# Kernel optimization log

Measured on AMD Instinct MI355X. Metric: run time of the kernel, lower is better.

The kernel has to match this reference:

```python
import jax, jax.numpy as jnp
import numpy as np

B, NCLS, T, D, L = 32, 20, 2048, 2048, 128
GAMMA = 0.1           # maxGamma temperature
THRES = 0.5           # lcs threshold
FEAT_MARGIN = 50.0
LAMB1, LAMB2, LAMB3 = 1.0, 5e-5, 2e-4
LAMB_LCS, LAMB_FSD = 0.1, 0.1


def _similarity(a, b):
    # row-normalized cosine similarity: [L, d] x [L, d] -> [L, L]
    a = a / jnp.linalg.norm(a, axis=1, keepdims=True)
    b = b / jnp.linalg.norm(b, axis=1, keepdims=True)
    return a @ b.T


def _fsd_dp(m, g):
    # soft-DP: C[i,j] = m[i-1,j-1] + gamma*logsumexp([C[i-1,j-1], g+C[i-1,j], g+C[i,j-1]]/gamma)
    n = m.shape[0]
    def row_step(prev_row, rows):          # prev_row: C[i-1, 0..n]
        m_row, g_row = rows
        def col_step(c_left, xs):
            c_diag, c_up, m_ij, g_ij = xs
            neigh = jnp.stack([c_diag, g_ij + c_up, g_ij + c_left])
            new = m_ij + GAMMA * jax.nn.logsumexp(neigh / GAMMA)
            return new, new
        _, vals = jax.lax.scan(col_step, jnp.zeros((), m.dtype),
                               (prev_row[:-1], prev_row[1:], m_row, g_row))
        new_row = jnp.concatenate([jnp.zeros((1,), m.dtype), vals])
        return new_row, None
    final_row, _ = jax.lax.scan(row_step, jnp.zeros((n + 1,), m.dtype), (m, g))
    return final_row[-1]


def _lcs_dp(s):
    # C[i,j] = C[i-1,j-1]+s if s>thres else max(C[i-1,j], C[i,j-1])
    n = s.shape[0]
    def row_step(prev_row, s_row):
        def col_step(c_left, xs):
            c_diag, c_up, s_ij = xs
            new = jnp.where(s_ij > THRES, c_diag + s_ij, jnp.maximum(c_up, c_left))
            return new, new
        _, vals = jax.lax.scan(col_step, jnp.zeros((), s.dtype),
                               (prev_row[:-1], prev_row[1:], s_row))
        return jnp.concatenate([jnp.zeros((1,), s.dtype), vals]), None
    final_row, _ = jax.lax.scan(row_step, jnp.zeros((n + 1,), s.dtype), s)
    return final_row[-1]


def _fsd_pair(c0, c1):
    h = c0.shape[-1] // 2
    m = _similarity(c0[:, :h], c1[:, :h])
    g = _similarity(c0[:, h:], c1[:, h:])
    return _fsd_dp(m, g)


def _lcs_pair(c0, c1):
    sim = _similarity(c0, c1)
    s = jnp.maximum(0.0, sim - 0.8) * 5.0
    return _lcs_dp(s)


def _cls_criterion(x, lab):
    return -jnp.mean(jnp.sum(jnp.log(x + 1e-45) * lab, axis=1))


def _acm_forward(act_inst_cls, act_cont_cls, act_back_cls, vid_label, temp_att,
                 act_inst_feat, act_cont_feat, act_back_feat, temp_cas,
                 lcs_candi, fsd_act_candi, fsd_bak_candi, pos_pair, neg_pair):
    bsz = act_inst_cls.shape[0]
    zeros = jnp.zeros((bsz, 1), act_inst_cls.dtype)
    ones = jnp.ones((bsz, 1), act_inst_cls.dtype)
    inst_lab = jnp.concatenate([vid_label, zeros], axis=1)
    cont_lab = jnp.concatenate([vid_label, ones], axis=1)
    back_lab = jnp.concatenate([jnp.zeros_like(vid_label), ones], axis=1)
    inst_lab = inst_lab / jnp.sum(inst_lab, axis=1, keepdims=True)
    cont_lab = cont_lab / jnp.sum(cont_lab, axis=1, keepdims=True)
    back_lab = back_lab / jnp.sum(back_lab, axis=1, keepdims=True)
    cls_loss = (_cls_criterion(act_inst_cls, inst_lab)
                + _cls_criterion(act_cont_cls, cont_lab)
                + _cls_criterion(act_back_cls, back_lab))

    guide_loss = jnp.mean(jnp.sum(jnp.abs(
        1.0 - temp_cas[:, :, -1] - jax.lax.stop_gradient(temp_att[:, :, 0])), axis=1))

    n_i = jnp.linalg.norm(act_inst_feat, axis=1)
    n_c = jnp.linalg.norm(act_cont_feat, axis=1)
    n_b = jnp.linalg.norm(act_back_feat, axis=1)
    f1 = jnp.maximum(FEAT_MARGIN - n_i + n_c, 0.0)
    f2 = jnp.maximum(FEAT_MARGIN - n_c + n_b, 0.0)
    feat_loss = jnp.mean((f1 + f2 + n_b) ** 2)

    sparse_loss = jnp.mean(jnp.sum(temp_att[:, :, :2], axis=1))

    acm_loss = cls_loss + LAMB1 * guide_loss + LAMB2 * feat_loss + LAMB3 * sparse_loss

    # LCS branch (pairs are constants)
    pos_lcs = jax.vmap(_lcs_pair)(lcs_candi[pos_pair[:, 0]], lcs_candi[pos_pair[:, 1]]).mean()
    neg_lcs = jax.vmap(_lcs_pair)(lcs_candi[neg_pair[:, 0]], lcs_candi[neg_pair[:, 1]]).mean()
    lcs_loss = neg_lcs - pos_lcs

    # FSD branch
    act_act = jax.vmap(_fsd_pair)(fsd_act_candi[pos_pair[:, 0]], fsd_act_candi[pos_pair[:, 1]]).mean()
    act_bak = jax.vmap(_fsd_pair)(fsd_act_candi[neg_pair[:, 0]], fsd_bak_candi[neg_pair[:, 1]]).mean()
    fsd_loss = act_bak - act_act

    return acm_loss + LAMB_LCS * lcs_loss + LAMB_FSD * fsd_loss


def setup_inputs() -> dict:
    key = jax.random.key(0)
    ks = jax.random.split(key, 12)
    # single-label videos: 16 classes, each appearing twice -> 16 pos pairs
    classes = np.arange(B) % 16
    vid_label = jnp.asarray(np.eye(NCLS, dtype=np.float32)[classes])
    pos_pair = jnp.asarray(np.stack([np.arange(16), np.arange(16) + 16], axis=1).astype(np.int32))
    neg_pair = jnp.asarray(np.stack([np.arange(16), np.arange(16) + 1], axis=1).astype(np.int32))
    return {
        "act_inst_cls": jax.random.uniform(ks[0], (B, NCLS + 1), jnp.float32),
        "act_cont_cls": jax.random.uniform(ks[1], (B, NCLS + 1), jnp.float32),
        "act_back_cls": jax.random.uniform(ks[2], (B, NCLS + 1), jnp.float32),
        "vid_label": vid_label,
        "temp_att": jax.random.uniform(ks[3], (B, T, 3), jnp.float32),
        "act_inst_feat": jax.random.normal(ks[4], (B, D), jnp.float32),
        "act_cont_feat": jax.random.normal(ks[5], (B, D), jnp.float32),
        "act_back_feat": jax.random.normal(ks[6], (B, D), jnp.float32),
        "temp_cas": jax.random.uniform(ks[7], (B, T, NCLS + 1), jnp.float32),
        "lcs_candi": jax.random.normal(ks[8], (B, L, D), jnp.float32),
        "fsd_act_candi": jax.random.normal(ks[9], (B, L, D), jnp.float32),
        "fsd_bak_candi": jax.random.normal(ks[10], (B, L, D), jnp.float32),
        "pos_pair": pos_pair,
        "neg_pair": neg_pair,
    }


def reference(act_inst_cls, act_cont_cls, act_back_cls, vid_label, temp_att,
              act_inst_feat, act_cont_feat, act_back_feat, temp_cas,
              lcs_candi, fsd_act_candi, fsd_bak_candi, pos_pair, neg_pair):
    return _acm_forward(act_inst_cls, act_cont_cls, act_back_cls, vid_label, temp_att,
                        act_inst_feat, act_cont_feat, act_back_feat, temp_cas,
                        lcs_candi, fsd_act_candi, fsd_bak_candi, pos_pair, neg_pair)
```

## Files before the change

kernel.cpp:

```cpp
#include <hip/hip_runtime.h>
#include <hip/hip_bf16.h>
#include <math.h>

#define B_    32
#define NCLS_ 20
#define T_    2048
#define D_    2048
#define L_    128
#define NPAIR 16

#define OFF_LCS_PART 0
#define OFF_M_PART   2097152
#define OFF_G_PART   3145728
#define OFF_RN       4194304
#define OFF_NFEAT    4214784
#define OFF_LCS_RES  4214880
#define OFF_FSD_RES  4214912
#define OFF_ACC      4214944
#define SLICE_STRIDE 524288

typedef __attribute__((ext_vector_type(8))) short bf16x8;
typedef __attribute__((ext_vector_type(4))) float f32x4;

__device__ __forceinline__ ushort f2bf(float f) {
    __hip_bfloat16 h = __float2bfloat16(f);
    return *reinterpret_cast<ushort*>(&h);
}

__global__ __launch_bounds__(64) void norm_guide_kernel(
        const float* __restrict__ lcs, const float* __restrict__ fa,
        const float* __restrict__ fb, const float* __restrict__ fi,
        const float* __restrict__ fc, const float* __restrict__ fbk,
        const float* __restrict__ att, const float* __restrict__ cas,
        float* __restrict__ ws) {
    __shared__ float sc[64 * 21 + 64 * 3];
    int b = blockIdx.x;
    int tid = threadIdx.x;

    if (b >= 20576) {
        float* sa = sc + 64 * 21;
        size_t e0 = (size_t)(b - 20576) * 64;
        const float4* pc = (const float4*)(cas + e0 * 21);
        #pragma unroll
        for (int i = 0; i < 6; ++i) {
            int idx = tid + i * 64;
            if (idx < 336) *(float4*)&sc[idx * 4] = pc[idx];
        }
        const float4* pa = (const float4*)(att + e0 * 3);
        if (tid < 48) *(float4*)&sa[tid * 4] = pa[tid];
        __syncthreads();
        float a0 = sa[tid * 3], a1 = sa[tid * 3 + 1];
        float g = fabsf(1.f - sc[tid * 21 + 20] - a0);
        float sp = a0 + a1;
        #pragma unroll
        for (int off = 32; off; off >>= 1) {
            g += __shfl_down(g, off);
            sp += __shfl_down(sp, off);
        }
        if (tid == 0) {
            atomicAdd(&ws[OFF_ACC + 0], g);
            atomicAdd(&ws[OFF_ACC + 1], sp);
        }
        return;
    }

    const float* src; float* dst; int len4; int recip = 1;
    float* rn = ws + OFF_RN;
    if (b < 4096) {
        src = lcs + (size_t)b * 2048; dst = rn + b; len4 = 512;
    } else if (b < 20480) {
        int region = (b - 4096) >> 12;
        int r = (b - 4096) & 4095;
        const float* base = (region < 2) ? fa : fb;
        src = base + (size_t)r * 2048 + (region & 1) * 1024;
        dst = rn + b; len4 = 256;
    } else {
        int r = b - 20480;
        const float* base = (r < 32) ? fi : (r < 64 ? fc : fbk);
        src = base + (size_t)(r & 31) * 2048;
        dst = ws + OFF_NFEAT + r; len4 = 512; recip = 0;
    }
    const float4* p = (const float4*)src;
    float s = 0.f;
    for (int i = tid; i < len4; i += 64) {
        float4 v = p[i];
        s += v.x * v.x + v.y * v.y + v.z * v.z + v.w * v.w;
    }
    #pragma unroll
    for (int off = 32; off; off >>= 1) s += __shfl_down(s, off);
    if (tid == 0) *dst = recip ? rsqrtf(s) : sqrtf(s);
}

__global__ __launch_bounds__(256) void sim_mfma_kernel(
        const float* __restrict__ lcs, const float* __restrict__ fa,
        const float* __restrict__ fb, const int* __restrict__ pos,
        const int* __restrict__ neg, float* __restrict__ ws) {
    int bid = blockIdx.x;
    const float *Aptr, *Bptr;
    float* out;

    if (bid < 128) {
        int job = bid >> 2, ks = bid & 3;
        int pi = job & 15;
        const int* pp = (job >= 16) ? neg : pos;
        int p0 = pp[2 * pi], p1 = pp[2 * pi + 1];
        Aptr = lcs + (size_t)p0 * L_ * D_ + ks * 512;
        Bptr = lcs + (size_t)p1 * L_ * D_ + ks * 512;
        out = ws + OFF_LCS_PART + ((size_t)ks * 32 + job) * 16384;
    } else {
        int e = bid - 128;
        int fj = e >> 1, ks = e & 1;
        int isneg = fj >= 32;
        int q = fj & 31;
        int pi = q >> 1, half = q & 1;
        const int* pp = isneg ? neg : pos;
        int p0 = pp[2 * pi], p1 = pp[2 * pi + 1];
        const float* Bbase = isneg ? fb : fa;
        Aptr = fa + (size_t)p0 * L_ * D_ + half * 1024 + ks * 512;
        Bptr = Bbase + (size_t)p1 * L_ * D_ + half * 1024 + ks * 512;
        int slot = (isneg ? 16 : 0) + pi;
        out = ws + (half ? OFF_G_PART : OFF_M_PART) + ((size_t)ks * 32 + slot) * 16384;
    }

    __shared__ ushort lA[2][128 * 64];
    __shared__ ushort lB[2][128 * 64];
    int tid = threadIdx.x;
    int lane = tid & 63;
    int w = tid >> 6;
    int wr = w >> 1, wc = w & 1;
    int lrow = lane & 15, lhk = lane >> 4;

    int srow[4], skb[4];
    #pragma unroll
    for (int i = 0; i < 4; ++i) {
        int c = tid + i * 256;
        srow[i] = c >> 3; skb[i] = c & 7;
    }

    float4 pa0[4], pa1[4], pb0[4], pb1[4];

    f32x4 acc[4][4];
    #pragma unroll
    for (int m = 0; m < 4; ++m)
        #pragma unroll
        for (int n = 0; n < 4; ++n)
            acc[m][n] = (f32x4){0.f, 0.f, 0.f, 0.f};

    #pragma unroll
    for (int i = 0; i < 4; ++i) {
        const float* sA = Aptr + (size_t)srow[i] * D_ + skb[i] * 8;
        pa0[i] = *(const float4*)sA; pa1[i] = *(const float4*)(sA + 4);
        const float* sB = Bptr + (size_t)srow[i] * D_ + skb[i] * 8;
        pb0[i] = *(const float4*)sB; pb1[i] = *(const float4*)(sB + 4);
    }
    #pragma unroll
    for (int i = 0; i < 4; ++i) {
        int idx = ((srow[i] * 64 + skb[i] * 8) ^ ((srow[i] & 7) << 3));
        bf16x8 sv, sw;
        sv[0] = (short)f2bf(pa0[i].x); sv[1] = (short)f2bf(pa0[i].y);
        sv[2] = (short)f2bf(pa0[i].z); sv[3] = (short)f2bf(pa0[i].w);
        sv[4] = (short)f2bf(pa1[i].x); sv[5] = (short)f2bf(pa1[i].y);
        sv[6] = (short)f2bf(pa1[i].z); sv[7] = (short)f2bf(pa1[i].w);
        *(bf16x8*)&lA[0][idx] = sv;
        sw[0] = (short)f2bf(pb0[i].x); sw[1] = (short)f2bf(pb0[i].y);
        sw[2] = (short)f2bf(pb0[i].z); sw[3] = (short)f2bf(pb0[i].w);
        sw[4] = (short)f2bf(pb1[i].x); sw[5] = (short)f2bf(pb1[i].y);
        sw[6] = (short)f2bf(pb1[i].z); sw[7] = (short)f2bf(pb1[i].w);
        *(bf16x8*)&lB[0][idx] = sw;
    }
    __syncthreads();

    #pragma unroll
    for (int t = 0; t < 8; ++t) {
        if (t < 7) {
            int k0 = (t + 1) * 64;
            #pragma unroll
            for (int i = 0; i < 4; ++i) {
                const float* sA = Aptr + (size_t)srow[i] * D_ + k0 + skb[i] * 8;
                pa0[i] = *(const float4*)sA; pa1[i] = *(const float4*)(sA + 4);
                const float* sB = Bptr + (size_t)srow[i] * D_ + k0 + skb[i] * 8;
                pb0[i] = *(const float4*)sB; pb1[i] = *(const float4*)(sB + 4);
            }
        }
        #pragma unroll
        for (int ks = 0; ks < 2; ++ks) {
            int kbase = ks * 32 + lhk * 8;
            bf16x8 afr[4], bfr[4];
            #pragma unroll
            for (int m = 0; m < 4; ++m) {
                int row = wr * 64 + m * 16 + lrow;
                int idx = ((row * 64 + kbase) ^ ((row & 7) << 3));
                afr[m] = *(const bf16x8*)&lA[t & 1][idx];
            }
            #pragma unroll
            for (int n = 0; n < 4; ++n) {
                int row = wc * 64 + n * 16 + lrow;
                int idx = ((row * 64 + kbase) ^ ((row & 7) << 3));
                bfr[n] = *(const bf16x8*)&lB[t & 1][idx];
            }
            #pragma unroll
            for (int m = 0; m < 4; ++m)
                #pragma unroll
                for (int n = 0; n < 4; ++n)
                    acc[m][n] = __builtin_amdgcn_mfma_f32_16x16x32_bf16(
                        afr[m], bfr[n], acc[m][n], 0, 0, 0);
        }
        if (t < 7) {
            #pragma unroll
            for (int i = 0; i < 4; ++i) {
                int idx = ((srow[i] * 64 + skb[i] * 8) ^ ((srow[i] & 7) << 3));
                bf16x8 sv, sw;
                sv[0] = (short)f2bf(pa0[i].x); sv[1] = (short)f2bf(pa0[i].y);
                sv[2] = (short)f2bf(pa0[i].z); sv[3] = (short)f2bf(pa0[i].w);
                sv[4] = (short)f2bf(pa1[i].x); sv[5] = (short)f2bf(pa1[i].y);
                sv[6] = (short)f2bf(pa1[i].z); sv[7] = (short)f2bf(pa1[i].w);
                *(bf16x8*)&lA[(t + 1) & 1][idx] = sv;
                sw[0] = (short)f2bf(pb0[i].x); sw[1] = (short)f2bf(pb0[i].y);
                sw[2] = (short)f2bf(pb0[i].z); sw[3] = (short)f2bf(pb0[i].w);
                sw[4] = (short)f2bf(pb1[i].x); sw[5] = (short)f2bf(pb1[i].y);
                sw[6] = (short)f2bf(pb1[i].z); sw[7] = (short)f2bf(pb1[i].w);
                *(bf16x8*)&lB[(t + 1) & 1][idx] = sw;
            }
        }
        __syncthreads();
    }

    #pragma unroll
    for (int m = 0; m < 4; ++m) {
        #pragma unroll
        for (int n = 0; n < 4; ++n) {
            int jj = wc * 64 + n * 16 + lrow;
            #pragma unroll
            for (int r = 0; r < 4; ++r) {
                int ii = wr * 64 + m * 16 + lhk * 4 + r;
                out[ii * L_ + jj] = acc[m][n][r];
            }
        }
    }
}

__global__ __launch_bounds__(256) void dp_kernel(const int* __restrict__ pos,
                                                 const int* __restrict__ neg,
                                                 float* __restrict__ ws) {
    __shared__ float Sm[128 * 128];
    __shared__ float Sg[128 * 128];
    int job = blockIdx.x;
    int tid = threadIdx.x;
    const float* rn = ws + OFF_RN;
    bool is_lcs = job < 32;

    if (is_lcs) {
        int pi = job & 15;
        const int* pp = (job >= 16) ? neg : pos;
        int p0 = pp[2 * pi], p1 = pp[2 * pi + 1];
        const float* P = ws + OFF_LCS_PART + (size_t)job * 16384;
        const float* rA = rn + p0 * 128;
        const float* rB = rn + p1 * 128;
        #pragma unroll
        for (int c = 0; c < 16; ++c) {
            int base = (c * 256 + tid) * 4;
            int r = base >> 7, j0 = base & 127;
            float4 v0 = *(const float4*)&P[base];
            float4 v1 = *(const float4*)&P[SLICE_STRIDE + base];
            float4 v2 = *(const float4*)&P[2 * SLICE_STRIDE + base];
            float4 v3 = *(const float4*)&P[3 * SLICE_STRIDE + base];
            float ra = rA[r];
            float4 rb = *(const float4*)&rB[j0];
            float4 sv;
            sv.x = fmaxf(((v0.x + v1.x + v2.x + v3.x) * ra * rb.x - 0.8f) * 5.f, 0.f);
            sv.y = fmaxf(((v0.y + v1.y + v2.y + v3.y) * ra * rb.y - 0.8f) * 5.f, 0.f);
            sv.z = fmaxf(((v0.z + v1.z + v2.z + v3.z) * ra * rb.z - 0.8f) * 5.f, 0.f);
            sv.w = fmaxf(((v0.w + v1.w + v2.w + v3.w) * ra * rb.w - 0.8f) * 5.f, 0.f);
            *(float4*)&Sm[base] = sv;
        }
    } else {
        int fj = job - 32;
        int isneg = fj >= 16;
        int pi = fj & 15;
        const int* pp = isneg ? neg : pos;
        int p0 = pp[2 * pi], p1 = pp[2 * pi + 1];
        const float* Pm = ws + OFF_M_PART + (size_t)fj * 16384;
        const float* Pg = ws + OFF_G_PART + (size_t)fj * 16384;
        const float* rAm = rn + 4096 + p0 * 128;
        const float* rBm = rn + (isneg ? 12288 : 4096) + p1 * 128;
        const float* rAg = rn + 8192 + p0 * 128;
        const float* rBg = rn + (isneg ? 16384 : 8192) + p1 * 128;
        #pragma unroll
        for (int c = 0; c < 16; ++c) {
            int base = (c * 256 + tid) * 4;
            int r = base >> 7, j0 = base & 127;
            float4 m0 = *(const float4*)&Pm[base];
            float4 m1 = *(const float4*)&Pm[SLICE_STRIDE + base];
            float4 g0 = *(const float4*)&Pg[base];
            float4 g1 = *(const float4*)&Pg[SLICE_STRIDE + base];
            float ram = rAm[r], rag = rAg[r];
            float4 rbm = *(const float4*)&rBm[j0];
            float4 rbg = *(const float4*)&rBg[j0];
            float4 mv, gv;
            mv.x = (m0.x + m1.x) * ram * rbm.x;
            mv.y = (m0.y + m1.y) * ram * rbm.y;
            mv.z = (m0.z + m1.z) * ram * rbm.z;
            mv.w = (m0.w + m1.w) * ram * rbm.w;
            gv.x = (g0.x + g1.x) * rag * rbg.x;
            gv.y = (g0.y + g1.y) * rag * rbg.y;
            gv.z = (g0.z + g1.z) * rag * rbg.z;
            gv.w = (g0.w + g1.w) * rag * rbg.w;
            *(float4*)&Sm[base] = mv;
            *(float4*)&Sg[base] = gv;
        }
    }
    __syncthreads();

    if (tid >= 64) return;
    int l = tid;
    const float* SA = Sm + l * 128;
    const float* SB = Sm + (64 + l) * 128;
    float a = 0.f, b = 0.f, ua_prev = 0.f, ub_prev = 0.f;

    if (is_lcs) {
        float sa_buf[4], sb_buf[4];
        #pragma unroll
        for (int p = 0; p < 4; ++p) {
            sa_buf[p] = SA[min(max(p - l, 0), 127)];
            sb_buf[p] = SB[min(max(p - 64 - l, 0), 127)];
        }
        #pragma unroll 4
        for (int t = 0; t < 256; ++t) {
            int slot = t & 3;
            float sa = sa_buf[slot], sb = sb_buf[slot];
            float ua = __shfl_up(a, 1);
            float a63 = __shfl(a, 63);
            float ub = __shfl_up(b, 1);
            if (l == 0) { ua = 0.f; ub = a63; }
            int ja = t - l, jb = t - 64 - l;
            float newa = (sa > 0.5f) ? (ua_prev + sa) : fmaxf(ua, a);
            float newb = (sb > 0.5f) ? (ub_prev + sb) : fmaxf(ub, b);
            if (ja >= 0 && ja < 128) a = newa;
            if (jb >= 0 && jb < 128) b = newb;
            ua_prev = ua; ub_prev = ub;
            sa_buf[slot] = SA[min(max(t + 4 - l, 0), 127)];
            sb_buf[slot] = SB[min(max(t + 4 - 64 - l, 0), 127)];
        }
        if (l == 63) ws[OFF_LCS_RES + job] = b;
    } else {
        const float* GA = Sg + l * 128;
        const float* GB = Sg + (64 + l) * 128;
        float mab[4], gab[4], mbb[4], gbb[4];
        #pragma unroll
        for (int p = 0; p < 4; ++p) {
            int ja = min(max(p - l, 0), 127), jb = min(max(p - 64 - l, 0), 127);
            mab[p] = SA[ja]; gab[p] = GA[ja];
            mbb[p] = SB[jb]; gbb[p] = GB[jb];
        }
        #pragma unroll 4
        for (int t = 0; t < 256; ++t) {
            int slot = t & 3;
            float ma = mab[slot], ga = gab[slot], mb = mbb[slot], gb = gbb[slot];
            float ua = __shfl_up(a, 1);
            float a63 = __shfl(a, 63);
            float ub = __shfl_up(b, 1);
            if (l == 0) { ua = 0.f; ub = a63; }
            int ja = t - l, jb = t - 64 - l;
            float x0 = ua_prev, x1 = ga + ua, x2 = ga + a;
            float mx = fmaxf(x0, fmaxf(x1, x2));
            float e0 = __expf((x0 - mx) * 10.f);
            float e1 = __expf((x1 - mx) * 10.f);
            float e2 = __expf((x2 - mx) * 10.f);
            float newa = ma + mx + 0.1f * __logf(e0 + e1 + e2);
            float y0 = ub_prev, y1 = gb + ub, y2 = gb + b;
            float my = fmaxf(y0, fmaxf(y1, y2));
            float f0 = __expf((y0 - my) * 10.f);
            float f1 = __expf((y1 - my) * 10.f);
            float f2 = __expf((y2 - my) * 10.f);
            float newb = mb + my + 0.1f * __logf(f0 + f1 + f2);
            if (ja >= 0 && ja < 128) a = newa;
            if (jb >= 0 && jb < 128) b = newb;
            ua_prev = ua; ub_prev = ub;
            int jan = min(max(t + 4 - l, 0), 127), jbn = min(max(t + 4 - 64 - l, 0), 127);
            mab[slot] = SA[jan]; gab[slot] = GA[jan];
            mbb[slot] = SB[jbn]; gbb[slot] = GB[jbn];
        }
        if (l == 63) ws[OFF_FSD_RES + (job - 32)] = b;
    }
}

__global__ __launch_bounds__(64) void final_kernel(const float* __restrict__ xi,
                                                   const float* __restrict__ xc,
                                                   const float* __restrict__ xb,
                                                   const float* __restrict__ vl,
                                                   const float* __restrict__ ws,
                                                   float* __restrict__ out) {
    const float* nfeat = ws + OFF_NFEAT;
    const float* lcs_res = ws + OFF_LCS_RES;
    const float* fsd_res = ws + OFF_FSD_RES;
    const float* acc = ws + OFF_ACC;
    int lane = threadIdx.x;
    float part = 0.f;

    if (lane < B_) {
        int b = lane;
        float sv = 0.f;
        for (int j = 0; j < NCLS_; ++j) sv += vl[b * NCLS_ + j];
        float inv_i = 1.f / sv;
        float inv_c = 1.f / (sv + 1.f);
        float si = 0.f, sc = 0.f;
        for (int j = 0; j < NCLS_; ++j) {
            float lab = vl[b * NCLS_ + j];
            if (lab != 0.f) {
                si += logf(xi[b * (NCLS_ + 1) + j] + 1e-45f) * lab * inv_i;
                sc += logf(xc[b * (NCLS_ + 1) + j] + 1e-45f) * lab * inv_c;
            }
        }
        sc += logf(xc[b * (NCLS_ + 1) + NCLS_] + 1e-45f) * inv_c;
        float sb = logf(xb[b * (NCLS_ + 1) + NCLS_] + 1e-45f);
        float cls = -(si + sc + sb) / (float)B_;

        float ni = nfeat[b], nc = nfeat[B_ + b], nb = nfeat[2 * B_ + b];
        float f1 = fmaxf(50.f - ni + nc, 0.f);
        float f2 = fmaxf(50.f - nc + nb, 0.f);
        float fv = f1 + f2 + nb;
        float feat = fv * fv / (float)B_;

        float sgn = (b < NPAIR) ? -1.f : 1.f;
        float lcs = sgn * lcs_res[b] / (float)NPAIR;
        float fsd = sgn * fsd_res[b] / (float)NPAIR;

        part = cls + 5e-5f * feat + 0.1f * (lcs + fsd);
    }
    #pragma unroll
    for (int off = 32; off; off >>= 1) part += __shfl_down(part, off);
    if (lane == 0) {
        float guide = acc[0] / (float)B_;
        float sparse = acc[1] / (float)B_;
        out[0] = part + guide + 2e-4f * sparse;
    }
}

extern "C" void kernel_launch(void* const* d_in, const int* in_sizes, int n_in,
                              void* d_out, int out_size, void* d_ws, size_t ws_size,
                              hipStream_t stream) {
    const float* act_inst_cls = (const float*)d_in[0];
    const float* act_cont_cls = (const float*)d_in[1];
    const float* act_back_cls = (const float*)d_in[2];
    const float* vid_label    = (const float*)d_in[3];
    const float* temp_att     = (const float*)d_in[4];
    const float* act_inst_feat= (const float*)d_in[5];
    const float* act_cont_feat= (const float*)d_in[6];
    const float* act_back_feat= (const float*)d_in[7];
    const float* temp_cas     = (const float*)d_in[8];
    const float* lcs_candi    = (const float*)d_in[9];
    const float* fsd_act      = (const float*)d_in[10];
    const float* fsd_bak      = (const float*)d_in[11];
    const int*   pos_pair     = (const int*)d_in[12];
    const int*   neg_pair     = (const int*)d_in[13];

    float* ws = (float*)d_ws;
    float* out = (float*)d_out;

    hipMemsetAsync(ws + OFF_ACC, 0, 2 * sizeof(float), stream);

    hipLaunchKernelGGL(sim_mfma_kernel, dim3(256), dim3(256), 0, stream,
                       lcs_candi, fsd_act, fsd_bak, pos_pair, neg_pair, ws);

    hipLaunchKernelGGL(norm_guide_kernel, dim3(21600), dim3(64), 0, stream,
                       lcs_candi, fsd_act, fsd_bak,
                       act_inst_feat, act_cont_feat, act_back_feat,
                       temp_att, temp_cas, ws);

    hipLaunchKernelGGL(dp_kernel, dim3(64), dim3(256), 0, stream,
                       pos_pair, neg_pair, ws);

    hipLaunchKernelGGL(final_kernel, dim3(1), dim3(64), 0, stream,
                       act_inst_cls, act_cont_cls, act_back_cls, vid_label,
                       ws, out);
}
```

Baseline: 269.7 us.

## Raise split-K factor for similarity GEMMs and use DPP shifts in DP wavefront

When the workspace is large enough, the similarity GEMM is split over twice as many K slices (8 for LCS, 4 for FSD). This doubles the number of blocks to fill more CUs, at the cost of more partial buffers for the DP kernel to read and sum. The DP wavefront loop now uses DPP row shifts and readlane in place of generic shuffles, and its LDS prefetch depth goes from 4 to 8 slots. Workspace offsets are now computed on the host from the split factors instead of fixed defines.

```diff
diff --git a/kernel.cpp b/kernel.cpp
--- a/kernel.cpp
+++ b/kernel.cpp
@@ -8,15 +8,6 @@
 #define D_    2048
 #define L_    128
 #define NPAIR 16
-
-#define OFF_LCS_PART 0
-#define OFF_M_PART   2097152
-#define OFF_G_PART   3145728
-#define OFF_RN       4194304
-#define OFF_NFEAT    4214784
-#define OFF_LCS_RES  4214880
-#define OFF_FSD_RES  4214912
-#define OFF_ACC      4214944
 #define SLICE_STRIDE 524288
 
 typedef __attribute__((ext_vector_type(8))) short bf16x8;
@@ -25,6 +16,24 @@
 __device__ __forceinline__ ushort f2bf(float f) {
     __hip_bfloat16 h = __float2bfloat16(f);
     return *reinterpret_cast<ushort*>(&h);
+}
+
+__device__ __forceinline__ float wave_shr1(float x) {
+#if __has_builtin(__builtin_amdgcn_update_dpp)
+    int r = __builtin_amdgcn_update_dpp(0, __builtin_bit_cast(int, x),
+                                        0x138 , 0xf, 0xf, true);
+    return __builtin_bit_cast(float, r);
+#else
+    return __shfl_up(x, 1);
+#endif
+}
+__device__ __forceinline__ float rdlane63(float x) {
+#if __has_builtin(__builtin_amdgcn_readlane)
+    return __builtin_bit_cast(float,
+        __builtin_amdgcn_readlane(__builtin_bit_cast(int, x), 63));
+#else
+    return __shfl(x, 63);
+#endif
 }
 
 __global__ __launch_bounds__(64) void norm_guide_kernel(
@@ -32,7 +41,8 @@
         const float* __restrict__ fb, const float* __restrict__ fi,
         const float* __restrict__ fc, const float* __restrict__ fbk,
         const float* __restrict__ att, const float* __restrict__ cas,
-        float* __restrict__ ws) {
+        float* __restrict__ rn, float* __restrict__ nfeat,
+        float* __restrict__ acc) {
     __shared__ float sc[64 * 21 + 64 * 3];
     int b = blockIdx.x;
     int tid = threadIdx.x;
@@ -58,14 +68,13 @@
             sp += __shfl_down(sp, off);
         }
         if (tid == 0) {
-            atomicAdd(&ws[OFF_ACC + 0], g);
-            atomicAdd(&ws[OFF_ACC + 1], sp);
+            atomicAdd(&acc[0], g);
+            atomicAdd(&acc[1], sp);
         }
         return;
     }
 
     const float* src; float* dst; int len4; int recip = 1;
-    float* rn = ws + OFF_RN;
     if (b < 4096) {
         src = lcs + (size_t)b * 2048; dst = rn + b; len4 = 512;
     } else if (b < 20480) {
@@ -78,7 +87,7 @@
         int r = b - 20480;
         const float* base = (r < 32) ? fi : (r < 64 ? fc : fbk);
         src = base + (size_t)(r & 31) * 2048;
-        dst = ws + OFF_NFEAT + r; len4 = 512; recip = 0;
+        dst = nfeat + r; len4 = 512; recip = 0;
     }
     const float4* p = (const float4*)src;
     float s = 0.f;
@@ -94,32 +103,39 @@
 __global__ __launch_bounds__(256) void sim_mfma_kernel(
         const float* __restrict__ lcs, const float* __restrict__ fa,
         const float* __restrict__ fb, const int* __restrict__ pos,
-        const int* __restrict__ neg, float* __restrict__ ws) {
+        const int* __restrict__ neg, float* __restrict__ lcs_part,
+        float* __restrict__ m_part, float* __restrict__ g_part,
+        int sl, int sf) {
     int bid = blockIdx.x;
     const float *Aptr, *Bptr;
     float* out;
-
-    if (bid < 128) {
-        int job = bid >> 2, ks = bid & 3;
+    int nst;
+
+    if (bid < 32 * sl) {
+        int job = bid / sl, ks = bid - job * sl;
+        int kofs = ks * (2048 / sl);
+        nst = 2048 / (64 * sl);
         int pi = job & 15;
         const int* pp = (job >= 16) ? neg : pos;
         int p0 = pp[2 * pi], p1 = pp[2 * pi + 1];
-        Aptr = lcs + (size_t)p0 * L_ * D_ + ks * 512;
-        Bptr = lcs + (size_t)p1 * L_ * D_ + ks * 512;
-        out = ws + OFF_LCS_PART + ((size_t)ks * 32 + job) * 16384;
+        Aptr = lcs + (size_t)p0 * L_ * D_ + kofs;
+        Bptr = lcs + (size_t)p1 * L_ * D_ + kofs;
+        out = lcs_part + ((size_t)ks * 32 + job) * 16384;
     } else {
-        int e = bid - 128;
-        int fj = e >> 1, ks = e & 1;
+        int e = bid - 32 * sl;
+        int fj = e / sf, ks = e - fj * sf;
+        int kofs = ks * (1024 / sf);
+        nst = 1024 / (64 * sf);
         int isneg = fj >= 32;
         int q = fj & 31;
         int pi = q >> 1, half = q & 1;
         const int* pp = isneg ? neg : pos;
         int p0 = pp[2 * pi], p1 = pp[2 * pi + 1];
         const float* Bbase = isneg ? fb : fa;
-        Aptr = fa + (size_t)p0 * L_ * D_ + half * 1024 + ks * 512;
-        Bptr = Bbase + (size_t)p1 * L_ * D_ + half * 1024 + ks * 512;
+        Aptr = fa + (size_t)p0 * L_ * D_ + half * 1024 + kofs;
+        Bptr = Bbase + (size_t)p1 * L_ * D_ + half * 1024 + kofs;
         int slot = (isneg ? 16 : 0) + pi;
-        out = ws + (half ? OFF_G_PART : OFF_M_PART) + ((size_t)ks * 32 + slot) * 16384;
+        out = (half ? g_part : m_part) + ((size_t)ks * 32 + slot) * 16384;
     }
 
     __shared__ ushort lA[2][128 * 64];
@@ -170,9 +186,8 @@
     }
     __syncthreads();
 
-    #pragma unroll
-    for (int t = 0; t < 8; ++t) {
-        if (t < 7) {
+    for (int t = 0; t < nst; ++t) {
+        if (t < nst - 1) {
             int k0 = (t + 1) * 64;
             #pragma unroll
             for (int i = 0; i < 4; ++i) {
@@ -205,7 +220,7 @@
                     acc[m][n] = __builtin_amdgcn_mfma_f32_16x16x32_bf16(
                         afr[m], bfr[n], acc[m][n], 0, 0, 0);
         }
-        if (t < 7) {
+        if (t < nst - 1) {
             #pragma unroll
             for (int i = 0; i < 4; ++i) {
                 int idx = ((srow[i] * 64 + skb[i] * 8) ^ ((srow[i] & 7) << 3));
@@ -239,38 +254,40 @@
     }
 }
 
-__global__ __launch_bounds__(256) void dp_kernel(const int* __restrict__ pos,
-                                                 const int* __restrict__ neg,
-                                                 float* __restrict__ ws) {
+__global__ __launch_bounds__(256) void dp_kernel(
+        const int* __restrict__ pos, const int* __restrict__ neg,
+        const float* __restrict__ lcs_part, const float* __restrict__ m_part,
+        const float* __restrict__ g_part, const float* __restrict__ rn,
+        float* __restrict__ lres, float* __restrict__ fres,
+        int sl, int sf) {
     __shared__ float Sm[128 * 128];
     __shared__ float Sg[128 * 128];
     int job = blockIdx.x;
     int tid = threadIdx.x;
-    const float* rn = ws + OFF_RN;
     bool is_lcs = job < 32;
 
     if (is_lcs) {
         int pi = job & 15;
         const int* pp = (job >= 16) ? neg : pos;
         int p0 = pp[2 * pi], p1 = pp[2 * pi + 1];
-        const float* P = ws + OFF_LCS_PART + (size_t)job * 16384;
+        const float* P = lcs_part + (size_t)job * 16384;
         const float* rA = rn + p0 * 128;
         const float* rB = rn + p1 * 128;
-        #pragma unroll
         for (int c = 0; c < 16; ++c) {
             int base = (c * 256 + tid) * 4;
             int r = base >> 7, j0 = base & 127;
-            float4 v0 = *(const float4*)&P[base];
-            float4 v1 = *(const float4*)&P[SLICE_STRIDE + base];
-            float4 v2 = *(const float4*)&P[2 * SLICE_STRIDE + base];
-            float4 v3 = *(const float4*)&P[3 * SLICE_STRIDE + base];
+            float4 sacc = {0.f, 0.f, 0.f, 0.f};
+            for (int s = 0; s < sl; ++s) {
+                float4 v = *(const float4*)&P[(size_t)s * SLICE_STRIDE + base];
+                sacc.x += v.x; sacc.y += v.y; sacc.z += v.z; sacc.w += v.w;
+            }
             float ra = rA[r];
             float4 rb = *(const float4*)&rB[j0];
             float4 sv;
-            sv.x = fmaxf(((v0.x + v1.x + v2.x + v3.x) * ra * rb.x - 0.8f) * 5.f, 0.f);
-            sv.y = fmaxf(((v0.y + v1.y + v2.y + v3.y) * ra * rb.y - 0.8f) * 5.f, 0.f);
-            sv.z = fmaxf(((v0.z + v1.z + v2.z + v3.z) * ra * rb.z - 0.8f) * 5.f, 0.f);
-            sv.w = fmaxf(((v0.w + v1.w + v2.w + v3.w) * ra * rb.w - 0.8f) * 5.f, 0.f);
+            sv.x = fmaxf((sacc.x * ra * rb.x - 0.8f) * 5.f, 0.f);
+            sv.y = fmaxf((sacc.y * ra * rb.y - 0.8f) * 5.f, 0.f);
+            sv.z = fmaxf((sacc.z * ra * rb.z - 0.8f) * 5.f, 0.f);
+            sv.w = fmaxf((sacc.w * ra * rb.w - 0.8f) * 5.f, 0.f);
             *(float4*)&Sm[base] = sv;
         }
     } else {
@@ -279,32 +296,30 @@
         int pi = fj & 15;
         const int* pp = isneg ? neg : pos;
         int p0 = pp[2 * pi], p1 = pp[2 * pi + 1];
-        const float* Pm = ws + OFF_M_PART + (size_t)fj * 16384;
-        const float* Pg = ws + OFF_G_PART + (size_t)fj * 16384;
+        const float* Pm = m_part + (size_t)fj * 16384;
+        const float* Pg = g_part + (size_t)fj * 16384;
         const float* rAm = rn + 4096 + p0 * 128;
         const float* rBm = rn + (isneg ? 12288 : 4096) + p1 * 128;
         const float* rAg = rn + 8192 + p0 * 128;
         const float* rBg = rn + (isneg ? 16384 : 8192) + p1 * 128;
-        #pragma unroll
         for (int c = 0; c < 16; ++c) {
             int base = (c * 256 + tid) * 4;
             int r = base >> 7, j0 = base & 127;
-            float4 m0 = *(const float4*)&Pm[base];
-            float4 m1 = *(const float4*)&Pm[SLICE_STRIDE + base];
-            float4 g0 = *(const float4*)&Pg[base];
-            float4 g1 = *(const float4*)&Pg[SLICE_STRIDE + base];
+            float4 macc = {0.f, 0.f, 0.f, 0.f}, gacc = {0.f, 0.f, 0.f, 0.f};
+            for (int s = 0; s < sf; ++s) {
+                float4 m = *(const float4*)&Pm[(size_t)s * SLICE_STRIDE + base];
+                float4 g = *(const float4*)&Pg[(size_t)s * SLICE_STRIDE + base];
+                macc.x += m.x; macc.y += m.y; macc.z += m.z; macc.w += m.w;
+                gacc.x += g.x; gacc.y += g.y; gacc.z += g.z; gacc.w += g.w;
+            }
             float ram = rAm[r], rag = rAg[r];
             float4 rbm = *(const float4*)&rBm[j0];
             float4 rbg = *(const float4*)&rBg[j0];
             float4 mv, gv;
-            mv.x = (m0.x + m1.x) * ram * rbm.x;
-            mv.y = (m0.y + m1.y) * ram * rbm.y;
-            mv.z = (m0.z + m1.z) * ram * rbm.z;
-            mv.w = (m0.w + m1.w) * ram * rbm.w;
-            gv.x = (g0.x + g1.x) * rag * rbg.x;
-            gv.y = (g0.y + g1.y) * rag * rbg.y;
-            gv.z = (g0.z + g1.z) * rag * rbg.z;
-            gv.w = (g0.w + g1.w) * rag * rbg.w;
+            mv.x = macc.x * ram * rbm.x; mv.y = macc.y * ram * rbm.y;
+            mv.z = macc.z * ram * rbm.z; mv.w = macc.w * ram * rbm.w;
+            gv.x = gacc.x * rag * rbg.x; gv.y = gacc.y * rag * rbg.y;
+            gv.z = gacc.z * rag * rbg.z; gv.w = gacc.w * rag * rbg.w;
             *(float4*)&Sm[base] = mv;
             *(float4*)&Sg[base] = gv;
         }
@@ -318,19 +333,19 @@
     float a = 0.f, b = 0.f, ua_prev = 0.f, ub_prev = 0.f;
 
     if (is_lcs) {
-        float sa_buf[4], sb_buf[4];
-        #pragma unroll
-        for (int p = 0; p < 4; ++p) {
+        float sa_buf[8], sb_buf[8];
+        #pragma unroll
+        for (int p = 0; p < 8; ++p) {
             sa_buf[p] = SA[min(max(p - l, 0), 127)];
             sb_buf[p] = SB[min(max(p - 64 - l, 0), 127)];
         }
-        #pragma unroll 4
+        #pragma unroll 8
         for (int t = 0; t < 256; ++t) {
-            int slot = t & 3;
+            int slot = t & 7;
             float sa = sa_buf[slot], sb = sb_buf[slot];
-            float ua = __shfl_up(a, 1);
-            float a63 = __shfl(a, 63);
-            float ub = __shfl_up(b, 1);
+            float ua = wave_shr1(a);
+            float ub = wave_shr1(b);
+            float a63 = rdlane63(a);
             if (l == 0) { ua = 0.f; ub = a63; }
             int ja = t - l, jb = t - 64 - l;
             float newa = (sa > 0.5f) ? (ua_prev + sa) : fmaxf(ua, a);
@@ -338,27 +353,27 @@
             if (ja >= 0 && ja < 128) a = newa;
             if (jb >= 0 && jb < 128) b = newb;
             ua_prev = ua; ub_prev = ub;
-            sa_buf[slot] = SA[min(max(t + 4 - l, 0), 127)];
-            sb_buf[slot] = SB[min(max(t + 4 - 64 - l, 0), 127)];
-        }
-        if (l == 63) ws[OFF_LCS_RES + job] = b;
+            sa_buf[slot] = SA[min(max(t + 8 - l, 0), 127)];
+            sb_buf[slot] = SB[min(max(t + 8 - 64 - l, 0), 127)];
+        }
+        if (l == 63) lres[job] = b;
     } else {
         const float* GA = Sg + l * 128;
         const float* GB = Sg + (64 + l) * 128;
-        float mab[4], gab[4], mbb[4], gbb[4];
-        #pragma unroll
-        for (int p = 0; p < 4; ++p) {
+        float mab[8], gab[8], mbb[8], gbb[8];
+        #pragma unroll
+        for (int p = 0; p < 8; ++p) {
             int ja = min(max(p - l, 0), 127), jb = min(max(p - 64 - l, 0), 127);
             mab[p] = SA[ja]; gab[p] = GA[ja];
             mbb[p] = SB[jb]; gbb[p] = GB[jb];
         }
-        #pragma unroll 4
+        #pragma unroll 8
         for (int t = 0; t < 256; ++t) {
-            int slot = t & 3;
+            int slot = t & 7;
             float ma = mab[slot], ga = gab[slot], mb = mbb[slot], gb = gbb[slot];
-            float ua = __shfl_up(a, 1);
-            float a63 = __shfl(a, 63);
-            float ub = __shfl_up(b, 1);
+            float ua = wave_shr1(a);
+            float ub = wave_shr1(b);
+            float a63 = rdlane63(a);
             if (l == 0) { ua = 0.f; ub = a63; }
             int ja = t - l, jb = t - 64 - l;
             float x0 = ua_prev, x1 = ga + ua, x2 = ga + a;
@@ -376,24 +391,20 @@
             if (ja >= 0 && ja < 128) a = newa;
             if (jb >= 0 && jb < 128) b = newb;
             ua_prev = ua; ub_prev = ub;
-            int jan = min(max(t + 4 - l, 0), 127), jbn = min(max(t + 4 - 64 - l, 0), 127);
+            int jan = min(max(t + 8 - l, 0), 127), jbn = min(max(t + 8 - 64 - l, 0), 127);
             mab[slot] = SA[jan]; gab[slot] = GA[jan];
             mbb[slot] = SB[jbn]; gbb[slot] = GB[jbn];
         }
-        if (l == 63) ws[OFF_FSD_RES + (job - 32)] = b;
-    }
-}
-
-__global__ __launch_bounds__(64) void final_kernel(const float* __restrict__ xi,
-                                                   const float* __restrict__ xc,
-                                                   const float* __restrict__ xb,
-                                                   const float* __restrict__ vl,
-                                                   const float* __restrict__ ws,
-                                                   float* __restrict__ out) {
-    const float* nfeat = ws + OFF_NFEAT;
-    const float* lcs_res = ws + OFF_LCS_RES;
-    const float* fsd_res = ws + OFF_FSD_RES;
-    const float* acc = ws + OFF_ACC;
+        if (l == 63) fres[job - 32] = b;
+    }
+}
+
+__global__ __launch_bounds__(64) void final_kernel(
+        const float* __restrict__ xi, const float* __restrict__ xc,
+        const float* __restrict__ xb, const float* __restrict__ vl,
+        const float* __restrict__ nfeat, const float* __restrict__ lcs_res,
+        const float* __restrict__ fsd_res, const float* __restrict__ acc,
+        float* __restrict__ out) {
     int lane = threadIdx.x;
     float part = 0.f;
 
@@ -457,20 +468,40 @@
     float* ws = (float*)d_ws;
     float* out = (float*)d_out;
 
-    hipMemsetAsync(ws + OFF_ACC, 0, 2 * sizeof(float), stream);
-
-    hipLaunchKernelGGL(sim_mfma_kernel, dim3(256), dim3(256), 0, stream,
-                       lcs_candi, fsd_act, fsd_bak, pos_pair, neg_pair, ws);
+    int sl, sf;
+    size_t part_floats;
+    if (ws_size >= (size_t)36 * 1024 * 1024) {
+        sl = 8; sf = 4;
+    } else {
+        sl = 4; sf = 2;
+    }
+    part_floats = (size_t)(sl + 2 * sf) * SLICE_STRIDE;
+
+    float* lcs_part = ws;
+    float* m_part   = ws + (size_t)sl * SLICE_STRIDE;
+    float* g_part   = m_part + (size_t)sf * SLICE_STRIDE;
+    float* rn       = ws + part_floats;
+    float* nfeat    = rn + 20480;
+    float* lres     = nfeat + 96;
+    float* fres     = lres + 32;
+    float* acc      = fres + 32;
+
+    hipMemsetAsync(acc, 0, 2 * sizeof(float), stream);
+
+    hipLaunchKernelGGL(sim_mfma_kernel, dim3(32 * sl + 64 * sf), dim3(256), 0, stream,
+                       lcs_candi, fsd_act, fsd_bak, pos_pair, neg_pair,
+                       lcs_part, m_part, g_part, sl, sf);
 
     hipLaunchKernelGGL(norm_guide_kernel, dim3(21600), dim3(64), 0, stream,
                        lcs_candi, fsd_act, fsd_bak,
                        act_inst_feat, act_cont_feat, act_back_feat,
-                       temp_att, temp_cas, ws);
+                       temp_att, temp_cas, rn, nfeat, acc);
 
     hipLaunchKernelGGL(dp_kernel, dim3(64), dim3(256), 0, stream,
-                       pos_pair, neg_pair, ws);
+                       pos_pair, neg_pair, lcs_part, m_part, g_part, rn,
+                       lres, fres, sl, sf);
 
     hipLaunchKernelGGL(final_kernel, dim3(1), dim3(64), 0, stream,
                        act_inst_cls, act_cont_cls, act_back_cls, vid_label,
-                       ws, out);
-}
+                       nfeat, lres, fres, acc, out);
+}
```

Result: no change. 269.8 us (+0.0%).
